# Kernel optimization log

Measured on AMD Instinct MI355X. Metric: run time of the kernel, lower is better.

## Reference

```python
import jax, jax.numpy as jnp
import numpy as np

BETA = 0.25  # codebook loss weight


def setup_inputs() -> dict:
    key = jax.random.key(0)
    k1, k2 = jax.random.split(key)
    B, C, D = 32768, 4096, 128
    x = jax.random.normal(k1, (B, D), dtype=jnp.float32)
    codes = jax.random.normal(k2, (1, C, D), dtype=jnp.float32)
    return {"x": x, "codes": codes}


def reference(x, codes):
    # x: (B, D), codes: (1, C, D). l2 metric, spherical_norm=False, STE training path
    # (dead-code reinit branch is a no-op on first forward since unused_count==0).
    c = codes[0]  # (C, D)
    x_sq = jnp.sum(x * x, axis=-1, keepdims=True)           # (B, 1)
    c_sq = jnp.sum(c * c, axis=-1)                          # (C,)
    xc = jnp.einsum('bd,cd->bc', x, c)                      # (B, C)
    distances = x_sq + c_sq[None, :] - 2.0 * xc             # (B, C)
    indices = jnp.argmin(distances, axis=-1)                # (B,)
    quantized = c[indices]                                  # (B, D) codebook gather
    # straight-through estimator output
    quantized_out = x + jax.lax.stop_gradient(quantized - x)
    # loss_commit: distance(x, stop_grad(q)); loss_codebook: distance(stop_grad(x), q)
    q_sg = jax.lax.stop_gradient(quantized)
    x_sg = jax.lax.stop_gradient(x)
    loss_commit = jnp.mean(jnp.sum((x - q_sg) ** 2, axis=-1))
    loss_codebook = jnp.mean(jnp.sum((x_sg - quantized) ** 2, axis=-1))
    loss = loss_commit + BETA * loss_codebook
    return quantized_out, indices, loss
```

## Files before the change

### kernel.cpp

```cpp
#include <hip/hip_runtime.h>
#include <float.h>

#define B_ROWS 32768
#define C_CODES 4096
#define DDIM 128
#define MB 256
#define NCHUNKS 4
#define CCHUNK 1024
#define NH 32
#define ROWB 256

typedef __attribute__((ext_vector_type(16))) float f32x16;
using half8 = __attribute__((ext_vector_type(8))) _Float16;
typedef unsigned int u32;
typedef unsigned short u16;
typedef unsigned long long u64;

__device__ __forceinline__ u16 f2h(float f) {
    return __builtin_bit_cast(u16, (_Float16)f);
}

__device__ __forceinline__ void gl2lds16(const void* g, void* l) {
    __builtin_amdgcn_global_load_lds(
        (const __attribute__((address_space(1))) u32*)g,
        (__attribute__((address_space(3))) u32*)l, 16, 0, 0);
}

__global__ void prep_codes(const float* __restrict__ codes, u16* __restrict__ Bbig,
                           float* __restrict__ csqh) {
    const int w = threadIdx.x >> 6, lane = threadIdx.x & 63;
    const int c = blockIdx.x * 4 + w;
    const float2 v = ((const float2*)(codes + (size_t)c * DDIM))[lane];
    ushort2 b; b.x = f2h(v.x); b.y = f2h(v.y);
    const int sw = (c & 15) << 4;
    *(ushort2*)((char*)Bbig + (size_t)c * ROWB + ((lane * 4) ^ sw)) = b;
    float s = v.x * v.x + v.y * v.y;
    #pragma unroll
    for (int off = 32; off; off >>= 1) s += __shfl_xor(s, off);
    if (lane == 0) csqh[c] = 0.5f * s;
}

__global__ void transpose_codes(const float* __restrict__ codes, float* __restrict__ codesT) {
    const int g = blockIdx.x * 256 + threadIdx.x;
    const int d = g & 127;
    const int cg = g >> 7;
    float buf[32];
    #pragma unroll
    for (int k = 0; k < 32; ++k)
        buf[k] = codes[(size_t)(cg * 32 + k) * DDIM + d];
    #pragma unroll
    for (int i = 0; i < 8; ++i) {
        float4 v;
        v.x = buf[i * 4]; v.y = buf[i * 4 + 1]; v.z = buf[i * 4 + 2]; v.w = buf[i * 4 + 3];
        *(float4*)&codesT[(size_t)d * C_CODES + cg * 32 + i * 4] = v;
    }
}

__global__ __launch_bounds__(512, 2)
void gemm_top2(const float* __restrict__ x, const u16* __restrict__ Bbig,
               const float* __restrict__ csqh,
               float* __restrict__ pb1, float* __restrict__ pb2,
               int* __restrict__ pi1, float* __restrict__ xsq2) {
    __shared__ char smem[65536 + 4096];
    char* const Astage = smem;
    float* const csq_l = (float*)(smem + 65536);

    const int tid = threadIdx.x;
    const int lane = tid & 63;
    const int w = tid >> 6;
    const int blkrow = blockIdx.x * MB;
    const int cbase = blockIdx.y * CCHUNK;

    if (tid < 256) {
        const float4 v = ((const float4*)(csqh + cbase))[tid];
        float4 n; n.x = -v.x; n.y = -v.y; n.z = -v.z; n.w = -v.w;
        ((float4*)csq_l)[tid] = n;
    }
    {
        const int r = tid >> 1, h = tid & 1;
        const float4* xp = (const float4*)(x + (size_t)(blkrow + r) * DDIM + h * 64);
        char* Arow = Astage + r * ROWB;
        const int sw = (r & 15) << 4;
        float ss = 0.f;
        #pragma unroll
        for (int i = 0; i < 16; ++i) {
            const float4 v = xp[i];
            ss += v.x * v.x + v.y * v.y + v.z * v.z + v.w * v.w;
            uint2 pk;
            pk.x = (u32)f2h(v.x) | ((u32)f2h(v.y) << 16);
            pk.y = (u32)f2h(v.z) | ((u32)f2h(v.w) << 16);
            *(uint2*)(Arow + ((h * 128 + i * 8) ^ sw)) = pk;
        }
        if (blockIdx.y == 0) xsq2[blkrow * 2 + tid] = ss;
    }
    __syncthreads();

    const int col0 = lane & 31;
    const int khalf = (lane >> 5) << 4;
    half8 afr[8];
    {
        const int arow = w * 32 + col0;
        const char* Ab = Astage + arow * ROWB;
        const int swa = (arow & 15) << 4;
        #pragma unroll
        for (int ks = 0; ks < 8; ++ks)
            afr[ks] = *(const half8*)(Ab + ((ks * 32 + khalf) ^ swa));
    }
    __syncthreads();

    {
        const char* src = (const char*)Bbig + (size_t)cbase * ROWB;
        gl2lds16(src +        tid * 16, smem +        tid * 16);
        gl2lds16(src + 8192 + tid * 16, smem + 8192 + tid * 16);
    }
    asm volatile("s_waitcnt vmcnt(1)" ::: "memory");
    __builtin_amdgcn_s_barrier();

    float b1v[16], b2v[16]; int b1i[16];
    #pragma unroll
    for (int r = 0; r < 16; ++r) { b1v[r] = -FLT_MAX; b2v[r] = -FLT_MAX; b1i[r] = 0; }

    const int swb = (col0 & 15) << 4;

    for (int h = 0; h < NH; ++h) {
        if (h + 2 < NH) {
            char* dbuf = smem + ((h + 2) & 3) * 8192;
            const char* src = (const char*)Bbig + (size_t)(cbase + (h + 2) * 32) * ROWB;
            gl2lds16(src + tid * 16, dbuf + tid * 16);
        }
        const char* Bl = smem + (h & 3) * 8192 + col0 * ROWB;

        const float cs0 = csq_l[h * 32 + col0];
        f32x16 acc;
        #pragma unroll
        for (int i = 0; i < 16; ++i) acc[i] = cs0;
        __builtin_amdgcn_s_setprio(1);
        #pragma unroll
        for (int ks = 0; ks < 8; ++ks) {
            const half8 bf = *(const half8*)(Bl + ((ks * 32 + khalf) ^ swb));
            acc = __builtin_amdgcn_mfma_f32_32x32x16_f16(afr[ks], bf, acc, 0, 0, 0);
        }
        __builtin_amdgcn_s_setprio(0);
        const int idx0 = cbase + h * 32 + col0;
        #pragma unroll
        for (int r = 0; r < 16; ++r) {
            const float s0 = acc[r];
            const float m2 = __builtin_amdgcn_fmed3f(b1v[r], b2v[r], s0);
            b1i[r] = (s0 > b1v[r]) ? idx0 : b1i[r];
            b1v[r] = fmaxf(b1v[r], s0);
            b2v[r] = m2;
        }
        if (h + 2 < NH) { asm volatile("s_waitcnt vmcnt(1)" ::: "memory"); }
        else            { asm volatile("s_waitcnt vmcnt(0)" ::: "memory"); }
        __builtin_amdgcn_s_barrier();
    }

    #pragma unroll
    for (int off = 1; off <= 16; off <<= 1) {
        #pragma unroll
        for (int r = 0; r < 16; ++r) {
            const float o1 = __shfl_xor(b1v[r], off);
            const int   oi = __shfl_xor(b1i[r], off);
            const float o2 = __shfl_xor(b2v[r], off);
            const float lo = fminf(b1v[r], o1);
            const float nb2 = fmaxf(lo, fmaxf(b2v[r], o2));
            const bool take = (o1 > b1v[r]) || (o1 == b1v[r] && oi < b1i[r]);
            if (take) { b1v[r] = o1; b1i[r] = oi; }
            b2v[r] = nb2;
        }
    }
    if (col0 == 0) {
        const int hi = lane >> 5;
        #pragma unroll
        for (int r = 0; r < 16; ++r) {
            const int rloc = w * 32 + (r & 3) + 8 * (r >> 2) + 4 * hi;
            const int grow = blkrow + rloc;
            const size_t o = (size_t)blockIdx.y * B_ROWS + grow;
            pb1[o] = b1v[r]; pb2[o] = b2v[r]; pi1[o] = b1i[r];
        }
    }
}

__global__ void select_flag(const float* __restrict__ pb1, const float* __restrict__ pb2,
                            const int* __restrict__ pi1, const float* __restrict__ xsq2,
                            int* __restrict__ idxf, int* __restrict__ list, int* __restrict__ cnt,
                            u64* __restrict__ amax64) {
    const int r = blockIdx.x * 256 + threadIdx.x;
    float b1 = pb1[r], b2 = pb2[r]; int bi = pi1[r];
    #pragma unroll
    for (int c = 1; c < NCHUNKS; ++c) {
        const float o1 = pb1[(size_t)c * B_ROWS + r], o2 = pb2[(size_t)c * B_ROWS + r];
        const int oi = pi1[(size_t)c * B_ROWS + r];
        const float lo = fminf(b1, o1);
        b2 = fmaxf(lo, fmaxf(b2, o2));
        const bool take = (o1 > b1) || (o1 == b1 && oi < bi);
        if (take) { b1 = o1; bi = oi; }
    }
    idxf[r] = bi;
    const float xsq = xsq2[2 * r] + xsq2[2 * r + 1];
    const float margin = 0.004f * sqrtf(xsq) + 0.008f;
    const bool flag = (b1 - b2) < margin;
    const unsigned long long m = __ballot(flag);
    const int lane = threadIdx.x & 63;
    int base = 0;
    const int nw = __popcll(m);
    if (lane == 0 && nw) base = atomicAdd(cnt, nw);
    base = __shfl(base, 0);
    if (flag) {
        const int pos = base + (int)__popcll(m & ((1ull << lane) - 1ull));
        list[pos] = r;
        amax64[pos] = 0ull;
    }
}

__global__ __launch_bounds__(256)
void recheck2(const float* __restrict__ x, const float* __restrict__ codesT,
              const float* __restrict__ csqh, const int* __restrict__ list,
              const int* __restrict__ cnt, u64* __restrict__ amax64) {
    __shared__ float xT[128][8];
    __shared__ u64 warr[4][8];
    const int tid = threadIdx.x;
    const int lane = tid & 63, w = tid >> 6;
    const int n = *cnt;
    if (n == 0) return;
    const int ntasks = ((n + 7) >> 3) << 3;

    for (int task = blockIdx.x; task < ntasks; task += gridDim.x) {
        const int slotbase = (task >> 3) << 3;
        const int ch = task & 7;
        __syncthreads();
        #pragma unroll
        for (int k = 0; k < 4; ++k) {
            const int i = tid + k * 256;
            const int d = i & 127, j = i >> 7;
            const int slot = min(slotbase + j, n - 1);
            xT[d][j] = x[(size_t)list[slot] * DDIM + d];
        }
        __syncthreads();

        const int c0 = ch * 512 + tid;
        const int c1 = c0 + 256;
        float acc[2][8][4];
        #pragma unroll
        for (int cc = 0; cc < 2; ++cc)
            #pragma unroll
            for (int r = 0; r < 8; ++r)
                #pragma unroll
                for (int p = 0; p < 4; ++p) acc[cc][r][p] = 0.f;

        for (int d4 = 0; d4 < 32; ++d4) {
            #pragma unroll
            for (int p = 0; p < 4; ++p) {
                const int d = d4 * 4 + p;
                const float cv0 = codesT[(size_t)d * C_CODES + c0];
                const float cv1 = codesT[(size_t)d * C_CODES + c1];
                const float4 xa = *(const float4*)&xT[d][0];
                const float4 xb = *(const float4*)&xT[d][4];
                acc[0][0][p] = fmaf(cv0, xa.x, acc[0][0][p]);
                acc[0][1][p] = fmaf(cv0, xa.y, acc[0][1][p]);
                acc[0][2][p] = fmaf(cv0, xa.z, acc[0][2][p]);
                acc[0][3][p] = fmaf(cv0, xa.w, acc[0][3][p]);
                acc[0][4][p] = fmaf(cv0, xb.x, acc[0][4][p]);
                acc[0][5][p] = fmaf(cv0, xb.y, acc[0][5][p]);
                acc[0][6][p] = fmaf(cv0, xb.z, acc[0][6][p]);
                acc[0][7][p] = fmaf(cv0, xb.w, acc[0][7][p]);
                acc[1][0][p] = fmaf(cv1, xa.x, acc[1][0][p]);
                acc[1][1][p] = fmaf(cv1, xa.y, acc[1][1][p]);
                acc[1][2][p] = fmaf(cv1, xa.z, acc[1][2][p]);
                acc[1][3][p] = fmaf(cv1, xa.w, acc[1][3][p]);
                acc[1][4][p] = fmaf(cv1, xb.x, acc[1][4][p]);
                acc[1][5][p] = fmaf(cv1, xb.y, acc[1][5][p]);
                acc[1][6][p] = fmaf(cv1, xb.z, acc[1][6][p]);
                acc[1][7][p] = fmaf(cv1, xb.w, acc[1][7][p]);
            }
        }

        const float cq0 = csqh[c0], cq1 = csqh[c1];
        #pragma unroll
        for (int r = 0; r < 8; ++r) {
            const float s0 = (acc[0][r][0] + acc[0][r][1]) + (acc[0][r][2] + acc[0][r][3]) - cq0;
            const float s1 = (acc[1][r][0] + acc[1][r][1]) + (acc[1][r][2] + acc[1][r][3]) - cq1;
            const float sb = (s1 > s0) ? s1 : s0;
            const int ib = (s1 > s0) ? c1 : c0;
            u32 su = __float_as_uint(sb);
            su ^= (sb < 0.f) ? 0xFFFFFFFFu : 0x80000000u;
            u64 key = ((u64)su << 32) | (u32)(4095 - ib);
            #pragma unroll
            for (int off = 1; off < 64; off <<= 1) {
                const u64 o = __shfl_xor(key, off);
                key = (o > key) ? o : key;
            }
            if (lane == 0) warr[w][r] = key;
        }
        __syncthreads();
        if (tid < 8) {
            const u64 k01 = warr[0][tid] > warr[1][tid] ? warr[0][tid] : warr[1][tid];
            const u64 k23 = warr[2][tid] > warr[3][tid] ? warr[2][tid] : warr[3][tid];
            const u64 k = k01 > k23 ? k01 : k23;
            atomicMax(&amax64[min(slotbase + tid, n - 1)], k);
        }
    }
}

__global__ void merge_flag(const int* __restrict__ list, const int* __restrict__ cnt,
                           const u64* __restrict__ amax64, int* __restrict__ idxf) {
    const int n = *cnt;
    for (int i = blockIdx.x * 256 + threadIdx.x; i < n; i += gridDim.x * 256)
        idxf[list[i]] = 4095 - (int)(amax64[i] & 0xFFFFFFFFull);
}

__global__ void finalize(const float* __restrict__ x, const float* __restrict__ codes,
                         const int* __restrict__ idxf, float* __restrict__ qout,
                         float* __restrict__ idxout, float* __restrict__ partials) {
    __shared__ float ls[4];
    const int w = threadIdx.x >> 6, lane = threadIdx.x & 63;
    const int rb = blockIdx.x * 16 + w * 4;
    float wsum = 0.f;
    #pragma unroll
    for (int j = 0; j < 4; ++j) {
        const int r = rb + j;
        const int bi = idxf[r];
        const float2 xv = ((const float2*)(x + (size_t)r * DDIM))[lane];
        const float2 cv = ((const float2*)(codes + (size_t)bi * DDIM))[lane];
        ((float2*)(qout + (size_t)r * DDIM))[lane] = cv;
        if (lane == 0) idxout[r] = (float)bi;
        const float dx = xv.x - cv.x, dy = xv.y - cv.y;
        wsum += dx * dx + dy * dy;
    }
    #pragma unroll
    for (int off = 32; off; off >>= 1) wsum += __shfl_xor(wsum, off);
    if (lane == 0) ls[w] = wsum;
    __syncthreads();
    if (threadIdx.x == 0) partials[blockIdx.x] = (ls[0] + ls[1]) + (ls[2] + ls[3]);
}

__global__ void loss_reduce(const float* __restrict__ partials, float* __restrict__ loss) {
    __shared__ float ls[4];
    const int tid = threadIdx.x, w = tid >> 6, lane = tid & 63;
    float s = 0.f;
    for (int i = tid; i < 2048; i += 256) s += partials[i];
    #pragma unroll
    for (int off = 32; off; off >>= 1) s += __shfl_xor(s, off);
    if (lane == 0) ls[w] = s;
    __syncthreads();
    if (tid == 0) *loss = ((ls[0] + ls[1]) + (ls[2] + ls[3])) * (1.25f / (float)B_ROWS);
}

extern "C" void kernel_launch(void* const* d_in, const int* in_sizes, int n_in,
                              void* d_out, int out_size, void* d_ws, size_t ws_size,
                              hipStream_t stream) {
    const float* x = (const float*)d_in[0];
    const float* codes = (const float*)d_in[1];

    float* out = (float*)d_out;
    float* qout = out;
    float* idxout = out + (size_t)B_ROWS * DDIM;
    float* loss = idxout + B_ROWS;

    float* codesT = qout;

    char* ws = (char*)d_ws;
    u16* Bbig     = (u16*)ws;
    float* csqh   = (float*)(ws + 1048576);
    float* pb1    = (float*)(ws + 1064960);
    float* pb2    = (float*)(ws + 1589248);
    int* pi1      = (int*)(ws + 2113536);
    float* xsq2   = (float*)(ws + 2637824);
    int* idxf     = (int*)(ws + 2899968);
    int* list     = (int*)(ws + 3031040);
    int* cnt      = (int*)(ws + 3162112);
    float* partials = (float*)(ws + 3162240);
    u64* amax64   = (u64*)(ws + 3170432);

    hipMemsetAsync(cnt, 0, 4, stream);
    prep_codes<<<C_CODES / 4, 256, 0, stream>>>(codes, Bbig, csqh);
    transpose_codes<<<64, 256, 0, stream>>>(codes, codesT);
    gemm_top2<<<dim3(B_ROWS / MB, NCHUNKS), 512, 0, stream>>>(x, Bbig, csqh, pb1, pb2, pi1, xsq2);
    select_flag<<<B_ROWS / 256, 256, 0, stream>>>(pb1, pb2, pi1, xsq2, idxf, list, cnt, amax64);
    recheck2<<<2048, 256, 0, stream>>>(x, codesT, csqh, list, cnt, amax64);
    merge_flag<<<64, 256, 0, stream>>>(list, cnt, amax64, idxf);
    finalize<<<B_ROWS / 16, 256, 0, stream>>>(x, codes, idxf, qout, idxout, partials);
    loss_reduce<<<1, 256, 0, stream>>>(partials, loss);
}
```

Measured before the change: 137.8 us.

## Load codebook fragments directly from global memory instead of LDS staging

The GEMM/top-2 kernel no longer stages codebook tiles through LDS with async global-to-LDS loads and per-iteration barriers. Each wave now reads its B fragments straight from global (L2-cached) memory, and the codebook prep drops the XOR swizzle. The block shrinks to 128 rows and 256 threads, with half the LDS, so more blocks can be resident. This removes barrier synchronisation between waves but puts every wave's B traffic on the global/L2 path, with latency the compiler must hide through unrolling.

After: 196.9 us. 42.9% more time.

```diff
diff --git a/kernel.cpp b/kernel.cpp
--- a/kernel.cpp
+++ b/kernel.cpp
@@ -4,7 +4,7 @@
 #define B_ROWS 32768
 #define C_CODES 4096
 #define DDIM 128
-#define MB 256
+#define MB 128
 #define NCHUNKS 4
 #define CCHUNK 1024
 #define NH 32
@@ -18,12 +18,6 @@
 
 __device__ __forceinline__ u16 f2h(float f) {
     return __builtin_bit_cast(u16, (_Float16)f);
-}
-
-__device__ __forceinline__ void gl2lds16(const void* g, void* l) {
-    __builtin_amdgcn_global_load_lds(
-        (const __attribute__((address_space(1))) u32*)g,
-        (__attribute__((address_space(3))) u32*)l, 16, 0, 0);
 }
 
 __global__ void prep_codes(const float* __restrict__ codes, u16* __restrict__ Bbig,
@@ -32,8 +26,7 @@
     const int c = blockIdx.x * 4 + w;
     const float2 v = ((const float2*)(codes + (size_t)c * DDIM))[lane];
     ushort2 b; b.x = f2h(v.x); b.y = f2h(v.y);
-    const int sw = (c & 15) << 4;
-    *(ushort2*)((char*)Bbig + (size_t)c * ROWB + ((lane * 4) ^ sw)) = b;
+    *(ushort2*)((char*)Bbig + (size_t)c * ROWB + lane * 4) = b;
     float s = v.x * v.x + v.y * v.y;
     #pragma unroll
     for (int off = 32; off; off >>= 1) s += __shfl_xor(s, off);
@@ -56,14 +49,14 @@
     }
 }
 
-__global__ __launch_bounds__(512, 2)
+__global__ __launch_bounds__(256, 2)
 void gemm_top2(const float* __restrict__ x, const u16* __restrict__ Bbig,
                const float* __restrict__ csqh,
                float* __restrict__ pb1, float* __restrict__ pb2,
                int* __restrict__ pi1, float* __restrict__ xsq2) {
-    __shared__ char smem[65536 + 4096];
+    __shared__ char smem[32768 + 4096];
     char* const Astage = smem;
-    float* const csq_l = (float*)(smem + 65536);
+    float* const csq_l = (float*)(smem + 32768);
 
     const int tid = threadIdx.x;
     const int lane = tid & 63;
@@ -71,7 +64,7 @@
     const int blkrow = blockIdx.x * MB;
     const int cbase = blockIdx.y * CCHUNK;
 
-    if (tid < 256) {
+    {
         const float4 v = ((const float4*)(csqh + cbase))[tid];
         float4 n; n.x = -v.x; n.y = -v.y; n.z = -v.z; n.w = -v.w;
         ((float4*)csq_l)[tid] = n;
@@ -106,41 +99,41 @@
         for (int ks = 0; ks < 8; ++ks)
             afr[ks] = *(const half8*)(Ab + ((ks * 32 + khalf) ^ swa));
     }
-    __syncthreads();
-
-    {
-        const char* src = (const char*)Bbig + (size_t)cbase * ROWB;
-        gl2lds16(src +        tid * 16, smem +        tid * 16);
-        gl2lds16(src + 8192 + tid * 16, smem + 8192 + tid * 16);
-    }
-    asm volatile("s_waitcnt vmcnt(1)" ::: "memory");
-    __builtin_amdgcn_s_barrier();
 
     float b1v[16], b2v[16]; int b1i[16];
     #pragma unroll
     for (int r = 0; r < 16; ++r) { b1v[r] = -FLT_MAX; b2v[r] = -FLT_MAX; b1i[r] = 0; }
 
-    const int swb = (col0 & 15) << 4;
-
+    const char* bbase = (const char*)Bbig + (size_t)(cbase + col0) * ROWB + khalf;
+
+    #pragma unroll 2
     for (int h = 0; h < NH; ++h) {
-        if (h + 2 < NH) {
-            char* dbuf = smem + ((h + 2) & 3) * 8192;
-            const char* src = (const char*)Bbig + (size_t)(cbase + (h + 2) * 32) * ROWB;
-            gl2lds16(src + tid * 16, dbuf + tid * 16);
-        }
-        const char* Bl = smem + (h & 3) * 8192 + col0 * ROWB;
+        const char* bl = bbase + h * (32 * ROWB);
+
+        half8 bf0 = *(const half8*)(bl + 0 * 32);
+        half8 bf1 = *(const half8*)(bl + 1 * 32);
+        half8 bf2 = *(const half8*)(bl + 2 * 32);
+        half8 bf3 = *(const half8*)(bl + 3 * 32);
+        half8 bf4 = *(const half8*)(bl + 4 * 32);
+        half8 bf5 = *(const half8*)(bl + 5 * 32);
+        half8 bf6 = *(const half8*)(bl + 6 * 32);
+        half8 bf7 = *(const half8*)(bl + 7 * 32);
 
         const float cs0 = csq_l[h * 32 + col0];
         f32x16 acc;
         #pragma unroll
         for (int i = 0; i < 16; ++i) acc[i] = cs0;
         __builtin_amdgcn_s_setprio(1);
-        #pragma unroll
-        for (int ks = 0; ks < 8; ++ks) {
-            const half8 bf = *(const half8*)(Bl + ((ks * 32 + khalf) ^ swb));
-            acc = __builtin_amdgcn_mfma_f32_32x32x16_f16(afr[ks], bf, acc, 0, 0, 0);
-        }
+        acc = __builtin_amdgcn_mfma_f32_32x32x16_f16(afr[0], bf0, acc, 0, 0, 0);
+        acc = __builtin_amdgcn_mfma_f32_32x32x16_f16(afr[1], bf1, acc, 0, 0, 0);
+        acc = __builtin_amdgcn_mfma_f32_32x32x16_f16(afr[2], bf2, acc, 0, 0, 0);
+        acc = __builtin_amdgcn_mfma_f32_32x32x16_f16(afr[3], bf3, acc, 0, 0, 0);
+        acc = __builtin_amdgcn_mfma_f32_32x32x16_f16(afr[4], bf4, acc, 0, 0, 0);
+        acc = __builtin_amdgcn_mfma_f32_32x32x16_f16(afr[5], bf5, acc, 0, 0, 0);
+        acc = __builtin_amdgcn_mfma_f32_32x32x16_f16(afr[6], bf6, acc, 0, 0, 0);
+        acc = __builtin_amdgcn_mfma_f32_32x32x16_f16(afr[7], bf7, acc, 0, 0, 0);
         __builtin_amdgcn_s_setprio(0);
+
         const int idx0 = cbase + h * 32 + col0;
         #pragma unroll
         for (int r = 0; r < 16; ++r) {
@@ -150,9 +143,6 @@
             b1v[r] = fmaxf(b1v[r], s0);
             b2v[r] = m2;
         }
-        if (h + 2 < NH) { asm volatile("s_waitcnt vmcnt(1)" ::: "memory"); }
-        else            { asm volatile("s_waitcnt vmcnt(0)" ::: "memory"); }
-        __builtin_amdgcn_s_barrier();
     }
 
     #pragma unroll
@@ -375,7 +365,7 @@
     hipMemsetAsync(cnt, 0, 4, stream);
     prep_codes<<<C_CODES / 4, 256, 0, stream>>>(codes, Bbig, csqh);
     transpose_codes<<<64, 256, 0, stream>>>(codes, codesT);
-    gemm_top2<<<dim3(B_ROWS / MB, NCHUNKS), 512, 0, stream>>>(x, Bbig, csqh, pb1, pb2, pi1, xsq2);
+    gemm_top2<<<dim3(B_ROWS / MB, NCHUNKS), 256, 0, stream>>>(x, Bbig, csqh, pb1, pb2, pi1, xsq2);
     select_flag<<<B_ROWS / 256, 256, 0, stream>>>(pb1, pb2, pi1, xsq2, idxf, list, cnt, amax64);
     recheck2<<<2048, 256, 0, stream>>>(x, codesT, csqh, list, cnt, amax64);
     merge_flag<<<64, 256, 0, stream>>>(list, cnt, amax64, idxf);
```
